# Kernel tuning notes

Hardware: AMD Instinct MI355X
Metric: run time of the kernel (lower is better)

The kernel has to match this reference:

```python
import jax, jax.numpy as jnp
import numpy as np
from jax.scipy.special import logsumexp

VOCAB, NLABEL, NSTATE = 32000, 16, 64
BATCH, MAXLEN = 512, 512


def setup_inputs() -> dict:
    key = jax.random.key(0)
    k1, k2, k3, k4, k5 = jax.random.split(key, 5)
    sentences = jax.random.randint(k1, (BATCH, MAXLEN), 0, VOCAB)
    length = jax.random.randint(k2, (BATCH,), 1, MAXLEN + 1)  # valid lengths in [1, MAXLEN]
    # parameters, uniform(-0.5, 0.5) as in reset_parameter()
    emb = jax.random.uniform(k3, (VOCAB, NSTATE), minval=-0.5, maxval=0.5, dtype=jnp.float32)
    transition = jax.random.uniform(k4, (NSTATE, NSTATE), minval=-0.5, maxval=0.5, dtype=jnp.float32)
    output = jax.random.uniform(k5, (NLABEL, NSTATE), minval=-0.5, maxval=0.5, dtype=jnp.float32)
    return {"sentences": sentences, "length": length, "emb": emb,
            "transition": transition, "output": output}


def reference(sentences, length, emb, transition, output):
    batch = sentences.shape[0]
    # emission log-probs per timestep: [T, B, S]
    emission = jax.nn.log_softmax(emb[sentences.T], axis=-1)
    trans = jax.nn.log_softmax(transition, axis=-1)  # [S, S]

    def step(f, e):
        # log-space matrix-vector product: logsumexp over previous state
        nf = logsumexp(trans[None, :, :] + f[:, None, :], axis=-1) + e  # [B, S]
        return nf, nf

    f0 = emission[0]
    _, rest = jax.lax.scan(step, f0, emission[1:])
    forwards = jnp.concatenate([f0[None], rest], axis=0)  # [T, B, S]
    hidden = forwards[length - 1, jnp.arange(batch)]  # [B, S]
    out_log = jax.nn.log_softmax(output, axis=-1)  # [L, S]
    score = logsumexp(out_log[None, :, :] + hidden[:, None, :], axis=-1)  # [B, L]
    return score
```

## Files before the change

kernel.cpp:

```cpp
#include <hip/hip_runtime.h>

#define VOCAB  32000
#define NSTATE 64
#define NLABEL 16
#define BATCH  512
#define MAXLEN 512

#define LOG2E 1.44269504088896340736f
#define LN2_D 0.69314718055994530942

#if defined(__has_builtin) && __has_builtin(__builtin_amdgcn_exp2f)
#define EXP2(x) __builtin_amdgcn_exp2f(x)
#else
#define EXP2(x) exp2f(x)
#endif
#if defined(__has_builtin) && __has_builtin(__builtin_amdgcn_logf)
#define LOG2(x) __builtin_amdgcn_logf(x)
#else
#define LOG2(x) log2f(x)
#endif

__device__ __forceinline__ float wave_max64(float x) {
#pragma unroll
  for (int off = 32; off > 0; off >>= 1) x = fmaxf(x, __shfl_xor(x, off, 64));
  return x;
}
__device__ __forceinline__ float wave_sum64(float x) {
#pragma unroll
  for (int off = 32; off > 0; off >>= 1) x += __shfl_xor(x, off, 64);
  return x;
}
__device__ __forceinline__ float bcast0(float x) {
  return __uint_as_float(__builtin_amdgcn_readfirstlane(__float_as_uint(x)));
}

__global__ void prep_emb_k(const float* __restrict__ emb, float* __restrict__ emb2) {
  const int w = blockIdx.x * 4 + (threadIdx.x >> 6);
  const int s = threadIdx.x & 63;
  const float v = emb[w * NSTATE + s] * LOG2E;
  const float m = wave_max64(v);
  const float ss = wave_sum64(EXP2(v - m));
  emb2[w * NSTATE + s] = v - m - LOG2(ss);
}

__global__ void prep_mats_k(const float* __restrict__ trans, const float* __restrict__ outp,
                            float* __restrict__ W, float* __restrict__ out2) {
  const int r = blockIdx.x, s = threadIdx.x;
  if (r < NSTATE) {
    const float v = trans[r * NSTATE + s] * LOG2E;
    const float m = wave_max64(v);
    const float ss = wave_sum64(EXP2(v - m));
    W[r * NSTATE + s] = EXP2(v - m - LOG2(ss));
  } else {
    const int l = r - NSTATE;
    const float v = outp[l * NSTATE + s] * LOG2E;
    const float m = wave_max64(v);
    const float ss = wave_sum64(EXP2(v - m));
    out2[l * NSTATE + s] = v - m - LOG2(ss);
  }
}

template <bool PRE>
__global__ __launch_bounds__(64) void iohmm_fwd(
    const int* __restrict__ sents, const int* __restrict__ length,
    const float* __restrict__ emb, const float* __restrict__ trans,
    const float* __restrict__ outp, const float* __restrict__ emb2,
    const float* __restrict__ W, const float* __restrict__ out2,
    float* __restrict__ score) {
  const int b = blockIdx.x;
  const int s = threadIdx.x;
  __shared__ __align__(16) float p_lds[2][NSTATE];
  __shared__ __align__(16) int s_ids[MAXLEN];

  {
    const int4* s4 = reinterpret_cast<const int4*>(sents + b * MAXLEN);
    int4 c0 = s4[s];
    int4 c1 = s4[64 + s];
    reinterpret_cast<int4*>(s_ids)[s] = c0;
    reinterpret_cast<int4*>(s_ids)[64 + s] = c1;
  }

  float wreg[NSTATE];
  if (PRE) {
#pragma unroll
    for (int j = 0; j < 16; ++j) {
      const float4 q = *reinterpret_cast<const float4*>(W + s * NSTATE + 4 * j);
      wreg[4 * j + 0] = q.x; wreg[4 * j + 1] = q.y;
      wreg[4 * j + 2] = q.z; wreg[4 * j + 3] = q.w;
    }
  } else {
#pragma unroll
    for (int j = 0; j < 16; ++j) {
      const float4 q = *reinterpret_cast<const float4*>(trans + s * NSTATE + 4 * j);
      wreg[4 * j + 0] = q.x * LOG2E; wreg[4 * j + 1] = q.y * LOG2E;
      wreg[4 * j + 2] = q.z * LOG2E; wreg[4 * j + 3] = q.w * LOG2E;
    }
    float m = -1e30f;
#pragma unroll
    for (int j = 0; j < NSTATE; ++j) m = fmaxf(m, wreg[j]);
    float ss = 0.f;
#pragma unroll
    for (int j = 0; j < NSTATE; ++j) ss += EXP2(wreg[j] - m);
    const float d = m + LOG2(ss);
#pragma unroll
    for (int j = 0; j < NSTATE; ++j) wreg[j] = EXP2(wreg[j] - d);
  }

  const int len = length[b];
  __syncthreads();

  const int w0 = s_ids[0];
  float f;
  if (PRE) {
    f = emb2[w0 * NSTATE + s];
  } else {
    const float v = emb[w0 * NSTATE + s] * LOG2E;
    const float dm = wave_max64(v);
    const float dsum = wave_sum64(EXP2(v - dm));
    f = v - dm - LOG2(dsum);
  }
  double MU = 0.0;

  int id1 = s_ids[1];
  float e_cur = PRE ? emb2[id1 * NSTATE + s] : emb[id1 * NSTATE + s] * LOG2E;
  int id_pref = s_ids[2];

  for (int t = 1; t < len; ++t) {
    const float e_nxt = PRE ? emb2[id_pref * NSTATE + s]
                            : emb[id_pref * NSTATE + s] * LOG2E;
    const int tpp = t + 2;
    const int id_nxt = s_ids[tpp < MAXLEN ? tpp : MAXLEN - 1];

    const float shift = bcast0(f);
    const float p = EXP2(f - shift);
    float* pb = p_lds[t & 1];
    pb[s] = p;
    __syncthreads();

    float a0 = 0.f, a1 = 0.f, a2 = 0.f, a3 = 0.f;
    float a4 = 0.f, a5 = 0.f, a6 = 0.f, a7 = 0.f;
#pragma unroll
    for (int j = 0; j < 8; ++j) {
      const float4 q0 = *reinterpret_cast<const float4*>(pb + 8 * j);
      const float4 q1 = *reinterpret_cast<const float4*>(pb + 8 * j + 4);
      a0 = fmaf(wreg[8 * j + 0], q0.x, a0);
      a1 = fmaf(wreg[8 * j + 1], q0.y, a1);
      a2 = fmaf(wreg[8 * j + 2], q0.z, a2);
      a3 = fmaf(wreg[8 * j + 3], q0.w, a3);
      a4 = fmaf(wreg[8 * j + 4], q1.x, a4);
      a5 = fmaf(wreg[8 * j + 5], q1.y, a5);
      a6 = fmaf(wreg[8 * j + 6], q1.z, a6);
      a7 = fmaf(wreg[8 * j + 7], q1.w, a7);
    }
    const float sum = ((a0 + a4) + (a1 + a5)) + ((a2 + a6) + (a3 + a7));

    float e;
    if (PRE) {
      e = e_cur;
    } else {
      const float dm = wave_max64(e_cur);
      const float dsum = wave_sum64(EXP2(e_cur - dm));
      e = e_cur - dm - LOG2(dsum);
    }
    f = LOG2(sum) + e;
    MU += (double)shift;

    e_cur = e_nxt;
    id_pref = id_nxt;
  }

  for (int l = 0; l < NLABEL; ++l) {
    float y;
    if (PRE) {
      y = out2[l * NSTATE + s] + f;
    } else {
      const float v = outp[l * NSTATE + s] * LOG2E;
      const float lm = wave_max64(v);
      const float lsum = wave_sum64(EXP2(v - lm));
      y = v - lm - LOG2(lsum) + f;
    }
    const float m = wave_max64(y);
    const float ssum = wave_sum64(EXP2(y - m));
    if (s == 0) {
      const double sc = MU + (double)m + (double)LOG2(ssum);
      score[b * NLABEL + l] = (float)(sc * LN2_D);
    }
  }
}

extern "C" void kernel_launch(void* const* d_in, const int* in_sizes, int n_in,
                              void* d_out, int out_size, void* d_ws, size_t ws_size,
                              hipStream_t stream) {
  const int* sents = (const int*)d_in[0];
  const int* length = (const int*)d_in[1];
  const float* emb = (const float*)d_in[2];
  const float* trans = (const float*)d_in[3];
  const float* outp = (const float*)d_in[4];
  float* score = (float*)d_out;

  const size_t emb2_bytes = (size_t)VOCAB * NSTATE * sizeof(float);
  const size_t W_off = emb2_bytes;
  const size_t out2_off = W_off + NSTATE * NSTATE * sizeof(float);
  const size_t need = out2_off + NLABEL * NSTATE * sizeof(float);

  if (ws_size >= need) {
    float* emb2 = (float*)d_ws;
    float* W = (float*)((char*)d_ws + W_off);
    float* out2 = (float*)((char*)d_ws + out2_off);
    prep_emb_k<<<VOCAB / 4, 256, 0, stream>>>(emb, emb2);
    prep_mats_k<<<NSTATE + NLABEL, 64, 0, stream>>>(trans, outp, W, out2);
    iohmm_fwd<true><<<BATCH, 64, 0, stream>>>(sents, length, emb, trans, outp,
                                              emb2, W, out2, score);
  } else {
    iohmm_fwd<false><<<BATCH, 64, 0, stream>>>(sents, length, emb, trans, outp,
                                               nullptr, nullptr, nullptr, score);
  }
}
```

Before: 296.3 us.

## Run forward recursion in linear space with periodic exponent rescaling and packed FMA

The forward recursion now carries probabilities in linear space. The next step's input is the matrix-vector sum times the exponentiated emission, so the per-step log2 and re-exponentiation leave the serial dependency chain. To avoid overflow and underflow, lane 0's float exponent is extracted every 16 steps and folded into an integer accumulator. The dot product uses packed two-wide FMA. The block barrier is replaced by an LDS waitcnt, relying on the block being a single 64-lane wavefront. In exchange it risks precision and range problems if values drift too far between rescales, and it depends on single-wave execution semantics.

```diff
diff --git a/kernel.cpp b/kernel.cpp
--- a/kernel.cpp
+++ b/kernel.cpp
@@ -1,4 +1,5 @@
 #include <hip/hip_runtime.h>
+#include <stdint.h>
 
 #define VOCAB  32000
 #define NSTATE 64
@@ -8,6 +9,8 @@
 
 #define LOG2E 1.44269504088896340736f
 #define LN2_D 0.69314718055994530942
+
+typedef float v2f __attribute__((ext_vector_type(2)));
 
 #if defined(__has_builtin) && __has_builtin(__builtin_amdgcn_exp2f)
 #define EXP2(x) __builtin_amdgcn_exp2f(x)
@@ -80,95 +83,118 @@
     reinterpret_cast<int4*>(s_ids)[64 + s] = c1;
   }
 
-  float wreg[NSTATE];
+  v2f w2[NSTATE / 2];
   if (PRE) {
 #pragma unroll
     for (int j = 0; j < 16; ++j) {
       const float4 q = *reinterpret_cast<const float4*>(W + s * NSTATE + 4 * j);
-      wreg[4 * j + 0] = q.x; wreg[4 * j + 1] = q.y;
-      wreg[4 * j + 2] = q.z; wreg[4 * j + 3] = q.w;
-    }
-  } else {
+      w2[2 * j + 0] = v2f{q.x, q.y};
+      w2[2 * j + 1] = v2f{q.z, q.w};
+    }
+  } else {
+    float wr[NSTATE];
 #pragma unroll
     for (int j = 0; j < 16; ++j) {
       const float4 q = *reinterpret_cast<const float4*>(trans + s * NSTATE + 4 * j);
-      wreg[4 * j + 0] = q.x * LOG2E; wreg[4 * j + 1] = q.y * LOG2E;
-      wreg[4 * j + 2] = q.z * LOG2E; wreg[4 * j + 3] = q.w * LOG2E;
+      wr[4 * j + 0] = q.x * LOG2E; wr[4 * j + 1] = q.y * LOG2E;
+      wr[4 * j + 2] = q.z * LOG2E; wr[4 * j + 3] = q.w * LOG2E;
     }
     float m = -1e30f;
 #pragma unroll
-    for (int j = 0; j < NSTATE; ++j) m = fmaxf(m, wreg[j]);
+    for (int j = 0; j < NSTATE; ++j) m = fmaxf(m, wr[j]);
     float ss = 0.f;
 #pragma unroll
-    for (int j = 0; j < NSTATE; ++j) ss += EXP2(wreg[j] - m);
+    for (int j = 0; j < NSTATE; ++j) ss += EXP2(wr[j] - m);
     const float d = m + LOG2(ss);
 #pragma unroll
-    for (int j = 0; j < NSTATE; ++j) wreg[j] = EXP2(wreg[j] - d);
+    for (int j = 0; j < NSTATE / 2; ++j)
+      w2[j] = v2f{EXP2(wr[2 * j] - d), EXP2(wr[2 * j + 1] - d)};
   }
 
   const int len = length[b];
   __syncthreads();
 
   const int w0 = s_ids[0];
-  float f;
+  float e0;
   if (PRE) {
-    f = emb2[w0 * NSTATE + s];
+    e0 = emb2[w0 * NSTATE + s];
   } else {
     const float v = emb[w0 * NSTATE + s] * LOG2E;
     const float dm = wave_max64(v);
     const float dsum = wave_sum64(EXP2(v - dm));
-    f = v - dm - LOG2(dsum);
-  }
-  double MU = 0.0;
-
-  int id1 = s_ids[1];
-  float e_cur = PRE ? emb2[id1 * NSTATE + s] : emb[id1 * NSTATE + s] * LOG2E;
+    e0 = v - dm - LOG2(dsum);
+  }
+  const float se0 = bcast0(e0);
+  float p = EXP2(e0 - se0);
+  double MU = (double)se0;
+  int MUi = 0;
+
+  const int id1 = s_ids[1];
+  float e_r = PRE ? emb2[id1 * NSTATE + s] : emb[id1 * NSTATE + s] * LOG2E;
   int id_pref = s_ids[2];
 
+#pragma unroll 2
   for (int t = 1; t < len; ++t) {
+    float* pb = p_lds[t & 1];
+    pb[s] = p;
+
     const float e_nxt = PRE ? emb2[id_pref * NSTATE + s]
                             : emb[id_pref * NSTATE + s] * LOG2E;
     const int tpp = t + 2;
     const int id_nxt = s_ids[tpp < MAXLEN ? tpp : MAXLEN - 1];
 
-    const float shift = bcast0(f);
-    const float p = EXP2(f - shift);
-    float* pb = p_lds[t & 1];
-    pb[s] = p;
-    __syncthreads();
-
-    float a0 = 0.f, a1 = 0.f, a2 = 0.f, a3 = 0.f;
-    float a4 = 0.f, a5 = 0.f, a6 = 0.f, a7 = 0.f;
-#pragma unroll
-    for (int j = 0; j < 8; ++j) {
-      const float4 q0 = *reinterpret_cast<const float4*>(pb + 8 * j);
-      const float4 q1 = *reinterpret_cast<const float4*>(pb + 8 * j + 4);
-      a0 = fmaf(wreg[8 * j + 0], q0.x, a0);
-      a1 = fmaf(wreg[8 * j + 1], q0.y, a1);
-      a2 = fmaf(wreg[8 * j + 2], q0.z, a2);
-      a3 = fmaf(wreg[8 * j + 3], q0.w, a3);
-      a4 = fmaf(wreg[8 * j + 4], q1.x, a4);
-      a5 = fmaf(wreg[8 * j + 5], q1.y, a5);
-      a6 = fmaf(wreg[8 * j + 6], q1.z, a6);
-      a7 = fmaf(wreg[8 * j + 7], q1.w, a7);
-    }
-    const float sum = ((a0 + a4) + (a1 + a5)) + ((a2 + a6) + (a3 + a7));
-
     float e;
     if (PRE) {
-      e = e_cur;
+      e = e_r;
     } else {
-      const float dm = wave_max64(e_cur);
-      const float dsum = wave_sum64(EXP2(e_cur - dm));
-      e = e_cur - dm - LOG2(dsum);
-    }
-    f = LOG2(sum) + e;
-    MU += (double)shift;
-
-    e_cur = e_nxt;
+      const float dm = wave_max64(e_r);
+      const float dsum = wave_sum64(EXP2(e_r - dm));
+      e = e_r - dm - LOG2(dsum);
+    }
+    const float se = bcast0(e);
+    const float q = EXP2(e - se);
+
+    asm volatile("s_waitcnt lgkmcnt(0)" ::: "memory");
+
+    const float4* pb4 = reinterpret_cast<const float4*>(pb);
+    v2f A0{0.f, 0.f}, A1 = A0, A2 = A0, A3 = A0, A4 = A0, A5 = A0, A6 = A0, A7 = A0;
+#pragma unroll
+    for (int j = 0; j < 4; ++j) {
+      const float4 qa = pb4[4 * j + 0];
+      const float4 qb = pb4[4 * j + 1];
+      const float4 qc = pb4[4 * j + 2];
+      const float4 qd = pb4[4 * j + 3];
+      A0 = __builtin_elementwise_fma(w2[8 * j + 0], v2f{qa.x, qa.y}, A0);
+      A1 = __builtin_elementwise_fma(w2[8 * j + 1], v2f{qa.z, qa.w}, A1);
+      A2 = __builtin_elementwise_fma(w2[8 * j + 2], v2f{qb.x, qb.y}, A2);
+      A3 = __builtin_elementwise_fma(w2[8 * j + 3], v2f{qb.z, qb.w}, A3);
+      A4 = __builtin_elementwise_fma(w2[8 * j + 4], v2f{qc.x, qc.y}, A4);
+      A5 = __builtin_elementwise_fma(w2[8 * j + 5], v2f{qc.z, qc.w}, A5);
+      A6 = __builtin_elementwise_fma(w2[8 * j + 6], v2f{qd.x, qd.y}, A6);
+      A7 = __builtin_elementwise_fma(w2[8 * j + 7], v2f{qd.z, qd.w}, A7);
+    }
+    const v2f S0 = A0 + A4, S1 = A1 + A5, S2 = A2 + A6, S3 = A3 + A7;
+    const v2f T0 = S0 + S2, T1 = S1 + S3;
+    const v2f U = T0 + T1;
+    const float sum = U.x + U.y;
+
+    p = sum * q;
+
+    if ((t & 15) == 0) {
+      const uint32_t u = __builtin_amdgcn_readfirstlane(__float_as_uint(p));
+      const int ex = (int)((u >> 23) & 255u) - 127;
+      const float r = __uint_as_float((uint32_t)(127 - ex) << 23);
+      p *= r;
+      MUi += ex;
+    }
+
+    MU += (double)se;
+    e_r = e_nxt;
     id_pref = id_nxt;
   }
 
+  const float f = LOG2(p);
+  const double MUt = MU + (double)MUi;
   for (int l = 0; l < NLABEL; ++l) {
     float y;
     if (PRE) {
@@ -182,7 +208,7 @@
     const float m = wave_max64(y);
     const float ssum = wave_sum64(EXP2(y - m));
     if (s == 0) {
-      const double sc = MU + (double)m + (double)LOG2(ssum);
+      const double sc = MUt + (double)m + (double)LOG2(ssum);
       score[b * NLABEL + l] = (float)(sc * LN2_D);
     }
   }
```

Result: faster. 261.4 us (-11.8%).
